# Kernel optimization log

Measured on AMD Instinct MI355X. Metric: run time of the kernel, lower is better.

## Reference

```python
import jax, jax.numpy as jnp
import numpy as np

N_NODES = 200000
N_EDGES = 6400000
NUM_FEATURES = 128


def _glorot(key, fan_in, fan_out):
    return jax.random.normal(key, (fan_in, fan_out), jnp.float32) * (1.0 / np.sqrt(fan_in))


def gcn_conv(x, src, dst, W, b):
    """PyG GCNConv: h = D^{-1/2}(A+I)D^{-1/2} (x @ W) + b, self-loops added."""
    n = x.shape[0]
    ones = jnp.ones(src.shape, x.dtype)
    # degree after adding self-loops: 1 + in-degree (edges flow src -> dst)
    deg = 1.0 + jax.ops.segment_sum(ones, dst, num_segments=n)
    dinv = jax.lax.rsqrt(deg)  # deg >= 1, safe
    h = x @ W  # [n, out]
    norm = dinv[src] * dinv[dst]  # [E]
    msg = h[src] * norm[:, None]
    agg = jax.ops.segment_sum(msg, dst, num_segments=n)
    agg = agg + h * (dinv * dinv)[:, None]  # self-loop contribution
    return agg + b


def setup_inputs() -> dict:
    key = jax.random.key(0)
    ks = jax.random.split(key, 16)
    x = jax.random.normal(ks[0], (N_NODES, NUM_FEATURES), jnp.float32)
    edge_index = jax.random.randint(ks[1], (2, N_EDGES), 0, N_NODES, dtype=jnp.int64)
    params = {
        'W1': _glorot(ks[2], NUM_FEATURES, 64), 'b1': jnp.zeros((64,), jnp.float32),
        'W2': _glorot(ks[3], 64, 32),           'b2': jnp.zeros((32,), jnp.float32),
        'W3': _glorot(ks[4], 32, 16),           'b3': jnp.zeros((16,), jnp.float32),
        'Wsk02': _glorot(ks[5], NUM_FEATURES, 32), 'bsk02': jnp.zeros((32,), jnp.float32),
        'Wsk13': _glorot(ks[6], 64, 16),           'bsk13': jnp.zeros((16,), jnp.float32),
        'Wlin': _glorot(ks[7], 16, 1),             'blin': jnp.zeros((1,), jnp.float32),
    }
    return {'x': x, 'edge_index': edge_index, **params}


def reference(x, edge_index, W1, b1, W2, b2, W3, b3, Wsk02, bsk02, Wsk13, bsk13, Wlin, blin):
    # Dropout is identity in eval mode.
    src, dst = edge_index[0], edge_index[1]
    h1 = jax.nn.relu(gcn_conv(x, src, dst, W1, b1))
    h2 = jax.nn.relu(gcn_conv(h1, src, dst, W2, b2) + x @ Wsk02 + bsk02)
    h3 = jax.nn.relu(gcn_conv(h2, src, dst, W3, b3) + h1 @ Wsk13 + bsk13)
    return jax.nn.sigmoid(h3 @ Wlin + blin)  # [N, 1]
```

## Files before the change

### kernel.cpp

```cpp
#include <hip/hip_runtime.h>
#include <hip/hip_fp16.h>
#include <math.h>

#define MAXB 1024
#define MAXCB 128
#define TILE1 8192
#define SCAT_T 512
#define EPT1 (TILE1 / SCAT_T)
#define LCAP 13568
#define GCHUNK 4096

typedef _Float16 f16x8 __attribute__((ext_vector_type(8)));
typedef float f32x4 __attribute__((ext_vector_type(4)));


__device__ __forceinline__ unsigned int pack_f16(float a, float b) {
    __half2 h = __floats2half2_rn(a, b);
    return *reinterpret_cast<unsigned int*>(&h);
}
__device__ __forceinline__ float f16_lo(unsigned int u) {
    __half2 h = *reinterpret_cast<__half2*>(&u);
    return __low2float(h);
}
__device__ __forceinline__ float f16_hi(unsigned int u) {
    __half2 h = *reinterpret_cast<__half2*>(&u);
    return __high2float(h);
}
__device__ __forceinline__ void acc8(float* a, uint4 u) {
    a[0] += f16_lo(u.x); a[1] += f16_hi(u.x);
    a[2] += f16_lo(u.y); a[3] += f16_hi(u.y);
    a[4] += f16_lo(u.z); a[5] += f16_hi(u.z);
    a[6] += f16_lo(u.w); a[7] += f16_hi(u.w);
}
__device__ __forceinline__ void unpack8(uint4 u, float* v) {
    v[0] = f16_lo(u.x); v[1] = f16_hi(u.x);
    v[2] = f16_lo(u.y); v[3] = f16_hi(u.y);
    v[4] = f16_lo(u.z); v[5] = f16_hi(u.z);
    v[6] = f16_lo(u.w); v[7] = f16_hi(u.w);
}
__device__ __forceinline__ uint4 h2add4(uint4 a, uint4 b) {
    const __half2* pa = reinterpret_cast<const __half2*>(&a);
    const __half2* pb = reinterpret_cast<const __half2*>(&b);
    uint4 r;
    __half2* pr = reinterpret_cast<__half2*>(&r);
#pragma unroll
    for (int i = 0; i < 4; i++) pr[i] = __hadd2(pa[i], pb[i]);
    return r;
}
__device__ __forceinline__ unsigned int pkadd(unsigned int a, unsigned int b) {
    __half2 r = __hadd2(*reinterpret_cast<__half2*>(&a), *reinterpret_cast<__half2*>(&b));
    return *reinterpret_cast<unsigned int*>(&r);
}


__device__ __forceinline__ bool detect64(const int* __restrict__ ei) {
    int lane = threadIdx.x & 63;
    unsigned long long m = __ballot(ei[2 * lane + 1] != 0);
    return m == 0ull;
}

__device__ __forceinline__ int load_src(const int* ei, int e, bool is64, int i) {
    return is64 ? ei[2 * i] : ei[i];
}
__device__ __forceinline__ int load_dst(const int* ei, int e, bool is64, int i) {
    return is64 ? ei[2 * e + 2 * i] : ei[e + i];
}


__global__ __launch_bounds__(256) void bin_count(const int* __restrict__ ei, int e,
                                                 int shift, int* __restrict__ gcnt) {
    __shared__ int h[MAXB];
    for (int i = threadIdx.x; i < MAXB; i += 256) h[i] = 0;
    bool is64 = detect64(ei);
    __syncthreads();
    int stride = gridDim.x * 256;
    for (int i = blockIdx.x * 256 + threadIdx.x; i < e; i += stride) {
        int d = load_dst(ei, e, is64, i);
        atomicAdd(&h[d >> shift], 1);
    }
    __syncthreads();
    for (int i = threadIdx.x; i < MAXB; i += 256)
        if (h[i]) atomicAdd(&gcnt[i], h[i]);
}


__global__ void bin_scan_init(const int* __restrict__ gcnt, int nb, int ncb,
                              int* __restrict__ base, int* __restrict__ gcursor,
                              int* __restrict__ gcur1) {
    __shared__ int sh[1024];
    __shared__ int ex[1024];
    int t = threadIdx.x;
    int v = (t < nb) ? gcnt[t] : 0;
    sh[t] = v;
    __syncthreads();
    for (int off = 1; off < 1024; off <<= 1) {
        int x = (t >= off) ? sh[t - off] : 0;
        __syncthreads();
        sh[t] += x;
        __syncthreads();
    }
    int excl = sh[t] - v;
    ex[t] = excl;
    if (t < nb) {
        base[t] = excl;
        gcursor[t] = excl;
        if (t == nb - 1) base[nb] = sh[t];
    }
    __syncthreads();
    if (t < ncb) gcur1[t] = ex[8 * t];
}


__global__ __launch_bounds__(SCAT_T) void scatter_coarse(const int* __restrict__ ei, int e,
                                                         int shift,
                                                         int* __restrict__ gcur1,
                                                         unsigned int* __restrict__ gpk1) {
    __shared__ int hist[MAXCB];
    __shared__ int lbase[MAXCB];
    __shared__ int delta[MAXCB];
    __shared__ int cur[MAXCB];
    __shared__ unsigned int sbuf[TILE1];
    __shared__ unsigned char sbkt[TILE1];
    __shared__ int sh[SCAT_T];

    const int t = threadIdx.x;
    const int pkshift = shift + 3;
    const int pkmask = (1 << pkshift) - 1;
    const bool is64 = detect64(ei);
    const int tile0 = blockIdx.x * TILE1;
    const int cnt = min(TILE1, e - tile0);

    for (int i = t; i < MAXCB; i += SCAT_T) hist[i] = 0;
    __syncthreads();

    unsigned int pk[EPT1];
    int bk[EPT1];
#pragma unroll
    for (int k = 0; k < EPT1; k++) {
        int g = tile0 + k * SCAT_T + t;
        bk[k] = -1;
        if (g < e) {
            int s = load_src(ei, e, is64, g);
            int d = load_dst(ei, e, is64, g);
            pk[k] = ((unsigned int)s << pkshift) | (unsigned int)(d & pkmask);
            bk[k] = d >> pkshift;
            atomicAdd(&hist[bk[k]], 1);
        }
    }
    __syncthreads();

    {
        int v = (t < MAXCB) ? hist[t] : 0;
        sh[t] = v;
        __syncthreads();
        for (int off = 1; off < SCAT_T; off <<= 1) {
            int x = (t >= off) ? sh[t - off] : 0;
            __syncthreads();
            sh[t] += x;
            __syncthreads();
        }
        if (t < MAXCB) lbase[t] = sh[t] - v;
    }
    __syncthreads();

    if (t < MAXCB) {
        int c = hist[t];
        if (c > 0) delta[t] = atomicAdd(&gcur1[t], c) - lbase[t];
        cur[t] = lbase[t];
    }
    __syncthreads();

#pragma unroll
    for (int k = 0; k < EPT1; k++) {
        if (bk[k] >= 0) {
            int p = atomicAdd(&cur[bk[k]], 1);
            sbuf[p] = pk[k];
            sbkt[p] = (unsigned char)bk[k];
        }
    }
    __syncthreads();

    for (int i = t; i < cnt; i += SCAT_T)
        gpk1[delta[sbkt[i]] + i] = sbuf[i];
}


__global__ __launch_bounds__(SCAT_T) void scatter_fine(const unsigned int* __restrict__ gpk1,
                                                       const int* __restrict__ base,
                                                       int nbkt, int shift,
                                                       int* __restrict__ gcursor,
                                                       unsigned int* __restrict__ gpk2) {
    __shared__ int hist[8];
    __shared__ int lbase[8];
    __shared__ int delta[8];
    __shared__ int cur[8];
    __shared__ unsigned int sbuf[TILE1];
    __shared__ unsigned char sbkt[TILE1];

    const int t = threadIdx.x;
    const int cb = blockIdx.x >> 3;
    const int s = blockIdx.x & 7;
    const int f0 = 8 * cb;
    const int fhiIdx = min(f0 + 8, nbkt);
    const int lo = base[f0];
    const int hi = base[fhiIdx];
    const int len = hi - lo;
    const int slo = lo + (int)((long long)len * s / 8);
    const int shi = lo + (int)((long long)len * (s + 1) / 8);

    for (int tile0 = slo; tile0 < shi; tile0 += TILE1) {
        const int cnt = min(TILE1, shi - tile0);
        if (t < 8) hist[t] = 0;
        __syncthreads();

        unsigned int pk[EPT1];
        int bk[EPT1];
#pragma unroll
        for (int k = 0; k < EPT1; k++) {
            int li = k * SCAT_T + t;
            bk[k] = -1;
            if (li < cnt) {
                pk[k] = gpk1[tile0 + li];
                bk[k] = (pk[k] >> shift) & 7;
                atomicAdd(&hist[bk[k]], 1);
            }
        }
        __syncthreads();

        if (t == 0) {
            int run = 0;
            for (int f = 0; f < 8; f++) { lbase[f] = run; run += hist[f]; }
        }
        __syncthreads();
        if (t < 8) {
            int c = hist[t];
            if (c > 0) delta[t] = atomicAdd(&gcursor[f0 + t], c) - lbase[t];
            cur[t] = lbase[t];
        }
        __syncthreads();

#pragma unroll
        for (int k = 0; k < EPT1; k++) {
            if (bk[k] >= 0) {
                int p = atomicAdd(&cur[bk[k]], 1);
                sbuf[p] = pk[k];
                sbkt[p] = (unsigned char)bk[k];
            }
        }
        __syncthreads();

        for (int i = t; i < cnt; i += SCAT_T)
            gpk2[delta[sbkt[i]] + i] = sbuf[i];
        __syncthreads();
    }
}


__global__ __launch_bounds__(256) void bucket_build(const unsigned int* __restrict__ gpk,
                                                    const int* __restrict__ base, int shift,
                                                    int n, int e, float* __restrict__ dinv,
                                                    int* __restrict__ row_ptr,
                                                    int* __restrict__ col) {
    __shared__ int lcol[LCAP];
    __shared__ int dc[MAXB];
    __shared__ int cur[MAXB];
    __shared__ int sh[256];
    const int t = threadIdx.x;
    const int b = blockIdx.x;
    const int pkshift = shift + 3;
    const int mask = (1 << shift) - 1;
    const int width = 1 << shift;
    const int node0 = b << shift;
    const int nc = min(width, n - node0);
    const int lo = base[b], hi = base[b + 1];
    const int ecnt = hi - lo;

    for (int i = t; i < width; i += 256) dc[i] = 0;
    __syncthreads();
    for (int j = lo + t; j < hi; j += 256)
        atomicAdd(&dc[gpk[j] & mask], 1);
    __syncthreads();
    {
        int b4 = t * 4;
        int v0 = (b4 + 0 < width) ? dc[b4 + 0] : 0;
        int v1 = (b4 + 1 < width) ? dc[b4 + 1] : 0;
        int v2 = (b4 + 2 < width) ? dc[b4 + 2] : 0;
        int v3 = (b4 + 3 < width) ? dc[b4 + 3] : 0;
        int s = v0 + v1 + v2 + v3;
        sh[t] = s;
        __syncthreads();
        for (int off = 1; off < 256; off <<= 1) {
            int x = (t >= off) ? sh[t - off] : 0;
            __syncthreads();
            sh[t] += x;
            __syncthreads();
        }
        int excl = sh[t] - s;
        int pf[4] = {excl, excl + v0, excl + v0 + v1, excl + v0 + v1 + v2};
        int vv[4] = {v0, v1, v2, v3};
#pragma unroll
        for (int q = 0; q < 4; q++) {
            int i = b4 + q;
            if (i < nc) {
                row_ptr[node0 + i] = lo + pf[q];
                dinv[node0 + i] = rsqrtf(1.0f + (float)vv[q]);
            }
            if (i < width) cur[i] = pf[q];
        }
    }
    if (b == gridDim.x - 1 && t == 0) row_ptr[n] = e;
    __syncthreads();

    if (ecnt <= LCAP) {
        for (int j = lo + t; j < hi; j += 256) {
            unsigned int v = gpk[j];
            int p = atomicAdd(&cur[v & mask], 1);
            lcol[p] = (int)(v >> pkshift);
        }
        __syncthreads();
        for (int j = t; j < ecnt; j += 256)
            col[lo + j] = lcol[j];
    } else {
        for (int j = lo + t; j < hi; j += 256) {
            unsigned int v = gpk[j];
            int p = atomicAdd(&cur[v & mask], 1);
            col[lo + p] = (int)(v >> pkshift);
        }
    }
}


__global__ void prep_w(const float* __restrict__ W1, const float* __restrict__ Wsk02,
                       const float* __restrict__ W2, const float* __restrict__ Wsk13,
                       const float* __restrict__ W3, unsigned short* __restrict__ wt) {
    int i = blockIdx.x * 256 + threadIdx.x;
    float v;
    if (i < 12288) {
        int c = i >> 7, k = i & 127;
        v = (c < 64) ? W1[k * 64 + c] : Wsk02[k * 32 + (c - 64)];
    } else if (i < 15360) {
        int j = i - 12288;
        int c = j >> 6, k = j & 63;
        v = (c < 32) ? W2[k * 32 + c] : Wsk13[k * 16 + (c - 32)];
    } else if (i < 15872) {
        int j = i - 15360;
        int c = j >> 5, k = j & 31;
        v = W3[k * 16 + c];
    } else return;
    wt[i] = (unsigned short)pack_f16(v, 0.f);
}


template <int K, int CO1, int CO2, bool AHALF>
__global__ __launch_bounds__(256) void gemm_mfma(const void* __restrict__ Av,
                                                 const unsigned short* __restrict__ wt,
                                                 const float* __restrict__ dinv,
                                                 unsigned int* __restrict__ out1,
                                                 unsigned int* __restrict__ out2, int n) {
    constexpr int N = CO1 + CO2;
    constexpr int NCT = N / 16;
    constexpr int NK = K / 32;
    constexpr int CHK = K / 8;
    constexpr int SWZ = (CHK - 1) < 15 ? (CHK - 1) : 15;
    __shared__ __align__(16) unsigned char Ash[64 * K * 2];
    __shared__ __align__(16) unsigned char Bsh[N * K * 2];

    const int t = threadIdx.x;
    const int row0 = blockIdx.x * 64;

    for (int i = t; i < 64 * CHK; i += 256) {
        int r = i / CHK, c = i % CHK;
        int row = row0 + r;
        uint4 w{0u, 0u, 0u, 0u};
        if (row < n) {
            if (AHALF) {
                w = *reinterpret_cast<const uint4*>(
                    (const unsigned short*)Av + (size_t)row * K + c * 8);
            } else {
                const float* xr = (const float*)Av + (size_t)row * K + c * 8;
                float4 p = *reinterpret_cast<const float4*>(xr);
                float4 q = *reinterpret_cast<const float4*>(xr + 4);
                w.x = pack_f16(p.x, p.y); w.y = pack_f16(p.z, p.w);
                w.z = pack_f16(q.x, q.y); w.w = pack_f16(q.z, q.w);
            }
        }
        int addr = i * 16;
        addr ^= ((r & SWZ) << 4);
        *reinterpret_cast<uint4*>(&Ash[addr]) = w;
    }
    for (int i = t; i < N * CHK; i += 256) {
        int cc = i / CHK;
        uint4 w = *reinterpret_cast<const uint4*>(&wt[(i / CHK) * K + (i % CHK) * 8]);
        int addr = i * 16;
        addr ^= ((cc & SWZ) << 4);
        *reinterpret_cast<uint4*>(&Bsh[addr]) = w;
    }
    __syncthreads();

    const int wv = t >> 6;
    const int lane = t & 63;
    const int lrow = wv * 16 + (lane & 15);
    const int kb = (lane >> 4) * 16;

    f16x8 afr[NK];
#pragma unroll
    for (int s = 0; s < NK; s++) {
        int addr = lrow * (2 * K) + s * 64 + kb;
        addr ^= ((lrow & SWZ) << 4);
        afr[s] = *reinterpret_cast<const f16x8*>(&Ash[addr]);
    }

    f32x4 acc[NCT];
#pragma unroll
    for (int ct = 0; ct < NCT; ct++) acc[ct] = f32x4{0.f, 0.f, 0.f, 0.f};

#pragma unroll
    for (int ct = 0; ct < NCT; ct++) {
        int cc = ct * 16 + (lane & 15);
#pragma unroll
        for (int s = 0; s < NK; s++) {
            int addr = cc * (2 * K) + s * 64 + kb;
            addr ^= ((cc & SWZ) << 4);
            f16x8 bfr = *reinterpret_cast<const f16x8*>(&Bsh[addr]);
            acc[ct] = __builtin_amdgcn_mfma_f32_16x16x32_f16(afr[s], bfr, acc[ct], 0, 0, 0);
        }
    }

    const int rbase = row0 + wv * 16 + (lane >> 4) * 4;
    const int cidx = lane & 15;
    float dn[4];
#pragma unroll
    for (int r = 0; r < 4; r++) dn[r] = (rbase + r < n) ? dinv[rbase + r] : 0.f;

#pragma unroll
    for (int ct = 0; ct < NCT; ct++) {
        int col = ct * 16 + cidx;
        if (col < CO1) {
#pragma unroll
            for (int r = 0; r < 4; r++) {
                float v = acc[ct][r] * dn[r];
                float o = __shfl_xor(v, 1);
                int row = rbase + r;
                if (!(lane & 1) && row < n)
                    out1[(size_t)row * (CO1 / 2) + ct * 8 + cidx / 2] = pack_f16(v, o);
            }
        } else if (CO2 > 0) {
#pragma unroll
            for (int r = 0; r < 4; r++) {
                float v = acc[ct][r];
                float o = __shfl_xor(v, 1);
                int row = rbase + r;
                if (!(lane & 1) && row < n)
                    out2[(size_t)row * (CO2 / 2) + (ct * 16 + cidx - CO1) / 2] =
                        pack_f16(v, o);
            }
        }
    }
}


template <int F, bool PACKOUT>
__global__ __launch_bounds__(256) void gather_combine(
    const uint4* __restrict__ hp4, const int* __restrict__ row_ptr,
    const int* __restrict__ col, const float* __restrict__ dinv,
    const float* __restrict__ bias, void* __restrict__ outv, int n) {
    constexpr int L = F / 8;
    constexpr int EPW = 64 / L;
    int wid = (blockIdx.x * blockDim.x + threadIdx.x) >> 6;
    int lane = threadIdx.x & 63;
    if (wid >= n) return;
    int s = lane / L;
    int el = lane % L;
    int start = row_ptr[wid];
    int end = row_ptr[wid + 1];

    float a[8] = {0.f, 0.f, 0.f, 0.f, 0.f, 0.f, 0.f, 0.f};
    const uint4 z4{0u, 0u, 0u, 0u};
    for (int j = start + s; j < end; j += 4 * EPW) {
        int j1 = j + EPW, j2 = j + 2 * EPW, j3 = j + 3 * EPW;
        bool v1 = j1 < end, v2 = j2 < end, v3 = j3 < end;
        int c0 = col[j];
        int c1 = col[v1 ? j1 : j];
        int c2 = col[v2 ? j2 : j];
        int c3 = col[v3 ? j3 : j];
        uint4 u0 = hp4[(size_t)c0 * L + el];
        uint4 u1 = hp4[(size_t)c1 * L + el];
        uint4 u2 = hp4[(size_t)c2 * L + el];
        uint4 u3 = hp4[(size_t)c3 * L + el];
        if (!v1) u1 = z4;
        if (!v2) u2 = z4;
        if (!v3) u3 = z4;
        uint4 t01 = h2add4(u0, u1);
        uint4 t23 = h2add4(u2, u3);
        acc8(a, h2add4(t01, t23));
    }

#pragma unroll
    for (int m = L; m < 64; m <<= 1) {
#pragma unroll
        for (int q = 0; q < 8; q++) a[q] += __shfl_xor(a[q], m);
    }

    if (lane < L) {
        float dn = dinv[wid];
        uint4 us = hp4[(size_t)wid * L + el];
        float v[8];
        unpack8(us, v);
        float4 b0 = *reinterpret_cast<const float4*>(&bias[8 * el]);
        float4 b1 = *reinterpret_cast<const float4*>(&bias[8 * el + 4]);
        float o[8];
        o[0] = dn * a[0] + v[0] * dn + b0.x;
        o[1] = dn * a[1] + v[1] * dn + b0.y;
        o[2] = dn * a[2] + v[2] * dn + b0.z;
        o[3] = dn * a[3] + v[3] * dn + b0.w;
        o[4] = dn * a[4] + v[4] * dn + b1.x;
        o[5] = dn * a[5] + v[5] * dn + b1.y;
        o[6] = dn * a[6] + v[6] * dn + b1.z;
        o[7] = dn * a[7] + v[7] * dn + b1.w;
#pragma unroll
        for (int q = 0; q < 8; q++) o[q] = fmaxf(o[q], 0.f);
        if (PACKOUT) {
            uint4 pk{pack_f16(o[0], o[1]), pack_f16(o[2], o[3]),
                     pack_f16(o[4], o[5]), pack_f16(o[6], o[7])};
            ((uint4*)outv)[(size_t)wid * L + el] = pk;
        } else {
            float* out = (float*)outv;
            float4 w0{o[0], o[1], o[2], o[3]};
            float4 w1{o[4], o[5], o[6], o[7]};
            *reinterpret_cast<float4*>(&out[(size_t)wid * F + 8 * el]) = w0;
            *reinterpret_cast<float4*>(&out[(size_t)wid * F + 8 * el + 4]) = w1;
        }
    }
}


template <int F, int T, bool FINAL, bool PACKOUT>
__global__ __launch_bounds__(256) void gather_tpn(
    const uint4* __restrict__ hp4, const int* __restrict__ row_ptr,
    const int* __restrict__ col, const float* __restrict__ dinv,
    const float* __restrict__ bias, const uint4* __restrict__ skh,
    const float* __restrict__ bsk, void* __restrict__ outv,
    const float* __restrict__ Wlin, const float* __restrict__ blin, int n) {
    constexpr int L = F / 8;
    constexpr int NPB = 256 / T;
    __shared__ int lcol[GCHUNK];
    const int t = threadIdx.x;
    const int sub = t & (T - 1);
    const int node0 = blockIdx.x * NPB;
    const int node = node0 + (t / T);
    const int hiN = min(node0 + NPB, n);
    const int lo = row_ptr[node0];
    const int hi = row_ptr[hiN];

    int start = 0, end = 0;
    if (node < n) { start = row_ptr[node]; end = row_ptr[node + 1]; }

    unsigned int acc[F / 2];
#pragma unroll
    for (int q = 0; q < F / 2; q++) acc[q] = 0u;

    for (int ch = lo; ch < hi; ch += GCHUNK) {
        int cnt = min(GCHUNK, hi - ch);
        __syncthreads();
        for (int i = t; i < cnt; i += 256) lcol[i] = col[ch + i];
        __syncthreads();
        int first = start + sub;
        if (first < ch) first += ((ch - first + T - 1) & ~(T - 1));
        int last = min(end, ch + cnt);
        int j = first;
        if (j < last) {
            uint4 u[L];
            {
                const uint4* rp = hp4 + (size_t)lcol[j - ch] * L;
#pragma unroll
                for (int w = 0; w < L; w++) u[w] = rp[w];
            }
            for (j += T; j < last; j += T) {
                uint4 v[L];
                const uint4* rq = hp4 + (size_t)lcol[j - ch] * L;
#pragma unroll
                for (int w = 0; w < L; w++) v[w] = rq[w];
#pragma unroll
                for (int w = 0; w < L; w++) {
                    acc[4 * w + 0] = pkadd(acc[4 * w + 0], u[w].x);
                    acc[4 * w + 1] = pkadd(acc[4 * w + 1], u[w].y);
                    acc[4 * w + 2] = pkadd(acc[4 * w + 2], u[w].z);
                    acc[4 * w + 3] = pkadd(acc[4 * w + 3], u[w].w);
                }
#pragma unroll
                for (int w = 0; w < L; w++) u[w] = v[w];
            }
#pragma unroll
            for (int w = 0; w < L; w++) {
                acc[4 * w + 0] = pkadd(acc[4 * w + 0], u[w].x);
                acc[4 * w + 1] = pkadd(acc[4 * w + 1], u[w].y);
                acc[4 * w + 2] = pkadd(acc[4 * w + 2], u[w].z);
                acc[4 * w + 3] = pkadd(acc[4 * w + 3], u[w].w);
            }
        }
    }

#pragma unroll
    for (int m = 1; m < T; m <<= 1) {
#pragma unroll
        for (int q = 0; q < F / 2; q++) {
            unsigned int o = (unsigned int)__shfl_xor((int)acc[q], m);
            acc[q] = pkadd(acc[q], o);
        }
    }

    if (node < n && sub == 0) {
        float dn = dinv[node];
        const uint4* sp = hp4 + (size_t)node * L;
        float o[F];
#pragma unroll
        for (int w = 0; w < L; w++) {
            uint4 u = sp[w];
            float sv[8];
            unpack8(u, sv);
#pragma unroll
            for (int q = 0; q < 8; q++) {
                int f = w * 8 + q;
                float av = (q & 1) ? f16_hi(acc[4 * w + (q >> 1)])
                                   : f16_lo(acc[4 * w + (q >> 1)]);
                o[f] = dn * (av + sv[q]) + bias[f];
            }
        }
        if (skh) {
            const uint4* skp = skh + (size_t)node * L;
#pragma unroll
            for (int w = 0; w < L; w++) {
                float sv2[8];
                unpack8(skp[w], sv2);
#pragma unroll
                for (int q = 0; q < 8; q++)
                    o[w * 8 + q] += sv2[q] + bsk[w * 8 + q];
            }
        }
#pragma unroll
        for (int f = 0; f < F; f++) o[f] = fmaxf(o[f], 0.f);

        if (FINAL) {
            float d = blin[0];
#pragma unroll
            for (int f = 0; f < F; f++) d += o[f] * Wlin[f];
            ((float*)outv)[node] = 1.0f / (1.0f + expf(-d));
        } else if (PACKOUT) {
            uint4* o4 = (uint4*)outv + (size_t)node * L;
#pragma unroll
            for (int w = 0; w < L; w++) {
                uint4 pk{pack_f16(o[w * 8 + 0], o[w * 8 + 1]),
                         pack_f16(o[w * 8 + 2], o[w * 8 + 3]),
                         pack_f16(o[w * 8 + 4], o[w * 8 + 5]),
                         pack_f16(o[w * 8 + 6], o[w * 8 + 7])};
                o4[w] = pk;
            }
        }
    }
}


extern "C" void kernel_launch(void* const* d_in, const int* in_sizes, int n_in,
                              void* d_out, int out_size, void* d_ws, size_t ws_size,
                              hipStream_t stream) {
    const float* x     = (const float*)d_in[0];
    const int*   ei    = (const int*)d_in[1];
    const float* W1    = (const float*)d_in[2];
    const float* b1    = (const float*)d_in[3];
    const float* W2    = (const float*)d_in[4];
    const float* b2    = (const float*)d_in[5];
    const float* W3    = (const float*)d_in[6];
    const float* b3    = (const float*)d_in[7];
    const float* Wsk02 = (const float*)d_in[8];
    const float* bsk02 = (const float*)d_in[9];
    const float* Wsk13 = (const float*)d_in[10];
    const float* bsk13 = (const float*)d_in[11];
    const float* Wlin  = (const float*)d_in[12];
    const float* blin  = (const float*)d_in[13];

    const int n = in_sizes[0] / 128;
    const int e = in_sizes[1] / 2;

    int shift = 8;
    while (((n + (1 << shift) - 1) >> shift) > MAXB) shift++;
    const int nbkt = (n + (1 << shift) - 1) >> shift;
    const int ncb = (nbkt + 7) / 8;

    char* p = (char*)d_ws;
    auto alloc = [&](size_t bytes) {
        void* r = (void*)p;
        p += (bytes + 255) / 256 * 256;
        return r;
    };
    int*   gcnt    = (int*)alloc(MAXB * 4);
    int*   base    = (int*)alloc((MAXB + 1) * 4);
    int*   gcursor = (int*)alloc(MAXB * 4);
    int*   gcur1   = (int*)alloc(MAXCB * 4);
    unsigned short* wt = (unsigned short*)alloc(15872 * 2);
    int*   row_ptr = (int*)alloc((size_t)(n + 1) * 4);
    float* dinv    = (float*)alloc((size_t)n * 4);
    int*   col     = (int*)alloc((size_t)e * 4);
    size_t h1b     = (size_t)e * 4 > (size_t)n * 128 ? (size_t)e * 4 : (size_t)n * 128;
    unsigned int* h1 = (unsigned int*)alloc(h1b);
    unsigned int* h2 = (unsigned int*)alloc((size_t)n * 64);
    unsigned int* sk02 = (unsigned int*)alloc((size_t)n * 64);
    unsigned int* sk13 = (unsigned int*)alloc((size_t)n * 32);
    size_t prebytes = (size_t)e * 4 > (size_t)n * 128 ? (size_t)e * 4 : (size_t)n * 128;
    unsigned int* preb = (unsigned int*)alloc(prebytes);
    unsigned int* gpk1 = h1;
    unsigned int* gpk2 = preb;

    auto cdiv = [](int a, int b) { return (a + b - 1) / b; };

    prep_w<<<62, 256, 0, stream>>>(W1, Wsk02, W2, Wsk13, W3, wt);

    hipMemsetAsync(gcnt, 0, MAXB * 4, stream);
    bin_count<<<1024, 256, 0, stream>>>(ei, e, shift, gcnt);
    bin_scan_init<<<1, 1024, 0, stream>>>(gcnt, nbkt, ncb, base, gcursor, gcur1);
    scatter_coarse<<<cdiv(e, TILE1), SCAT_T, 0, stream>>>(ei, e, shift, gcur1, gpk1);
    scatter_fine<<<ncb * 8, SCAT_T, 0, stream>>>(gpk1, base, nbkt, shift, gcursor, gpk2);
    bucket_build<<<nbkt, 256, 0, stream>>>(gpk2, base, shift, n, e, dinv, row_ptr, col);

    gemm_mfma<128, 64, 32, false><<<cdiv(n, 64), 256, 0, stream>>>(
        x, wt, dinv, preb, sk02, n);
    gather_combine<64, true><<<cdiv(n, 4), 256, 0, stream>>>(
        (const uint4*)preb, row_ptr, col, dinv, b1, h1, n);

    gemm_mfma<64, 32, 16, true><<<cdiv(n, 64), 256, 0, stream>>>(
        h1, wt + 12288, dinv, preb, sk13, n);
    gather_tpn<32, 8, false, true><<<cdiv(n, 32), 256, 0, stream>>>(
        (const uint4*)preb, row_ptr, col, dinv, b2, (const uint4*)sk02, bsk02,
        h2, nullptr, nullptr, n);

    gemm_mfma<32, 16, 0, true><<<cdiv(n, 64), 256, 0, stream>>>(
        h2, wt + 15360, dinv, preb, sk13, n);
    gather_tpn<16, 8, true, false><<<cdiv(n, 32), 256, 0, stream>>>(
        (const uint4*)preb, row_ptr, col, dinv, b3, (const uint4*)sk13, bsk13,
        d_out, Wlin, blin, n);
}
```

Measured before the change: 448.7 us.

## Replace two-level CSR bucketing with single coarse pass and fuse weight prep

Drops the fine scatter pass and builds CSR directly from coarse buckets of 2048+ nodes, each handled by one 1024-thread block that counts degrees, scans, and scatters columns using shared-memory cursors. Weight conversion is folded into the bin_count launch as extra blocks, removing one kernel launch. This removes a full read/write pass over the edge array but leaves ~98 blocks doing scattered global writes of col without local staging, so parallelism is lower and write locality is worse.

```diff
diff --git a/kernel.cpp b/kernel.cpp
--- a/kernel.cpp
+++ b/kernel.cpp
@@ -2,13 +2,13 @@
 #include <hip/hip_fp16.h>
 #include <math.h>
 
-#define MAXB 1024
 #define MAXCB 128
+#define MAXW 4096
 #define TILE1 8192
 #define SCAT_T 512
 #define EPT1 (TILE1 / SCAT_T)
-#define LCAP 13568
 #define GCHUNK 4096
+#define CNT_BLKS 1024
 
 typedef _Float16 f16x8 __attribute__((ext_vector_type(8)));
 typedef float f32x4 __attribute__((ext_vector_type(4)));
@@ -68,51 +68,70 @@
 
 
 __global__ __launch_bounds__(256) void bin_count(const int* __restrict__ ei, int e,
-                                                 int shift, int* __restrict__ gcnt) {
-    __shared__ int h[MAXB];
-    for (int i = threadIdx.x; i < MAXB; i += 256) h[i] = 0;
+                                                 int cshift, int* __restrict__ gcnt,
+                                                 const float* __restrict__ W1,
+                                                 const float* __restrict__ Wsk02,
+                                                 const float* __restrict__ W2,
+                                                 const float* __restrict__ Wsk13,
+                                                 const float* __restrict__ W3,
+                                                 unsigned short* __restrict__ wt) {
+    if (blockIdx.x >= CNT_BLKS) {
+        int i = (blockIdx.x - CNT_BLKS) * 256 + threadIdx.x;
+        float v;
+        if (i < 12288) {
+            int c = i >> 7, k = i & 127;
+            v = (c < 64) ? W1[k * 64 + c] : Wsk02[k * 32 + (c - 64)];
+        } else if (i < 15360) {
+            int j = i - 12288;
+            int c = j >> 6, k = j & 63;
+            v = (c < 32) ? W2[k * 32 + c] : Wsk13[k * 16 + (c - 32)];
+        } else if (i < 15872) {
+            int j = i - 15360;
+            int c = j >> 5, k = j & 31;
+            v = W3[k * 16 + c];
+        } else return;
+        wt[i] = (unsigned short)pack_f16(v, 0.f);
+        return;
+    }
+    __shared__ int h[MAXCB];
+    for (int i = threadIdx.x; i < MAXCB; i += 256) h[i] = 0;
     bool is64 = detect64(ei);
     __syncthreads();
-    int stride = gridDim.x * 256;
+    int stride = CNT_BLKS * 256;
     for (int i = blockIdx.x * 256 + threadIdx.x; i < e; i += stride) {
         int d = load_dst(ei, e, is64, i);
-        atomicAdd(&h[d >> shift], 1);
-    }
-    __syncthreads();
-    for (int i = threadIdx.x; i < MAXB; i += 256)
+        atomicAdd(&h[d >> cshift], 1);
+    }
+    __syncthreads();
+    for (int i = threadIdx.x; i < MAXCB; i += 256)
         if (h[i]) atomicAdd(&gcnt[i], h[i]);
 }
 
 
-__global__ void bin_scan_init(const int* __restrict__ gcnt, int nb, int ncb,
-                              int* __restrict__ base, int* __restrict__ gcursor,
-                              int* __restrict__ gcur1) {
-    __shared__ int sh[1024];
-    __shared__ int ex[1024];
+__global__ void bin_scan_init(const int* __restrict__ gcnt, int ncb,
+                              int* __restrict__ cbase, int* __restrict__ gcur1) {
+    __shared__ int sh[MAXCB];
     int t = threadIdx.x;
-    int v = (t < nb) ? gcnt[t] : 0;
+    int v = (t < ncb) ? gcnt[t] : 0;
     sh[t] = v;
     __syncthreads();
-    for (int off = 1; off < 1024; off <<= 1) {
+    for (int off = 1; off < MAXCB; off <<= 1) {
         int x = (t >= off) ? sh[t - off] : 0;
         __syncthreads();
         sh[t] += x;
         __syncthreads();
     }
-    int excl = sh[t] - v;
-    ex[t] = excl;
-    if (t < nb) {
-        base[t] = excl;
-        gcursor[t] = excl;
-        if (t == nb - 1) base[nb] = sh[t];
-    }
-    __syncthreads();
-    if (t < ncb) gcur1[t] = ex[8 * t];
+    if (t < ncb) {
+        int excl = sh[t] - v;
+        cbase[t] = excl;
+        gcur1[t] = excl;
+        if (t == ncb - 1) cbase[ncb] = sh[t];
+    }
 }
 
 
 __global__ __launch_bounds__(SCAT_T) void scatter_coarse(const int* __restrict__ ei, int e,
-                                                         int shift,
+                                                         int cshift,
                                                          int* __restrict__ gcur1,
                                                          unsigned int* __restrict__ gpk1) {
     __shared__ int hist[MAXCB];
@@ -124,8 +143,7 @@
     __shared__ int sh[SCAT_T];
 
     const int t = threadIdx.x;
-    const int pkshift = shift + 3;
-    const int pkmask = (1 << pkshift) - 1;
+    const int pkmask = (1 << cshift) - 1;
     const bool is64 = detect64(ei);
     const int tile0 = blockIdx.x * TILE1;
     const int cnt = min(TILE1, e - tile0);
@@ -142,8 +160,8 @@
         if (g < e) {
             int s = load_src(ei, e, is64, g);
             int d = load_dst(ei, e, is64, g);
-            pk[k] = ((unsigned int)s << pkshift) | (unsigned int)(d & pkmask);
-            bk[k] = d >> pkshift;
+            pk[k] = ((unsigned int)s << cshift) | (unsigned int)(d & pkmask);
+            bk[k] = d >> cshift;
             atomicAdd(&hist[bk[k]], 1);
         }
     }
@@ -185,169 +203,65 @@
 }
 
 
-__global__ __launch_bounds__(SCAT_T) void scatter_fine(const unsigned int* __restrict__ gpk1,
-                                                       const int* __restrict__ base,
-                                                       int nbkt, int shift,
-                                                       int* __restrict__ gcursor,
-                                                       unsigned int* __restrict__ gpk2) {
-    __shared__ int hist[8];
-    __shared__ int lbase[8];
-    __shared__ int delta[8];
-    __shared__ int cur[8];
-    __shared__ unsigned int sbuf[TILE1];
-    __shared__ unsigned char sbkt[TILE1];
-
-    const int t = threadIdx.x;
-    const int cb = blockIdx.x >> 3;
-    const int s = blockIdx.x & 7;
-    const int f0 = 8 * cb;
-    const int fhiIdx = min(f0 + 8, nbkt);
-    const int lo = base[f0];
-    const int hi = base[fhiIdx];
-    const int len = hi - lo;
-    const int slo = lo + (int)((long long)len * s / 8);
-    const int shi = lo + (int)((long long)len * (s + 1) / 8);
-
-    for (int tile0 = slo; tile0 < shi; tile0 += TILE1) {
-        const int cnt = min(TILE1, shi - tile0);
-        if (t < 8) hist[t] = 0;
-        __syncthreads();
-
-        unsigned int pk[EPT1];
-        int bk[EPT1];
-#pragma unroll
-        for (int k = 0; k < EPT1; k++) {
-            int li = k * SCAT_T + t;
-            bk[k] = -1;
-            if (li < cnt) {
-                pk[k] = gpk1[tile0 + li];
-                bk[k] = (pk[k] >> shift) & 7;
-                atomicAdd(&hist[bk[k]], 1);
-            }
-        }
-        __syncthreads();
-
-        if (t == 0) {
-            int run = 0;
-            for (int f = 0; f < 8; f++) { lbase[f] = run; run += hist[f]; }
-        }
-        __syncthreads();
-        if (t < 8) {
-            int c = hist[t];
-            if (c > 0) delta[t] = atomicAdd(&gcursor[f0 + t], c) - lbase[t];
-            cur[t] = lbase[t];
-        }
-        __syncthreads();
-
-#pragma unroll
-        for (int k = 0; k < EPT1; k++) {
-            if (bk[k] >= 0) {
-                int p = atomicAdd(&cur[bk[k]], 1);
-                sbuf[p] = pk[k];
-                sbkt[p] = (unsigned char)bk[k];
-            }
-        }
-        __syncthreads();
-
-        for (int i = t; i < cnt; i += SCAT_T)
-            gpk2[delta[sbkt[i]] + i] = sbuf[i];
-        __syncthreads();
-    }
-}
-
-
-__global__ __launch_bounds__(256) void bucket_build(const unsigned int* __restrict__ gpk,
-                                                    const int* __restrict__ base, int shift,
-                                                    int n, int e, float* __restrict__ dinv,
-                                                    int* __restrict__ row_ptr,
-                                                    int* __restrict__ col) {
-    __shared__ int lcol[LCAP];
-    __shared__ int dc[MAXB];
-    __shared__ int cur[MAXB];
-    __shared__ int sh[256];
+__global__ __launch_bounds__(1024) void bucket_build_coarse(
+    const unsigned int* __restrict__ gpk, const int* __restrict__ cbase,
+    int cshift, int n, int e, float* __restrict__ dinv,
+    int* __restrict__ row_ptr, int* __restrict__ col) {
+    __shared__ int dc[MAXW];
+    __shared__ int cur[MAXW];
+    __shared__ int sh[1024];
     const int t = threadIdx.x;
     const int b = blockIdx.x;
-    const int pkshift = shift + 3;
-    const int mask = (1 << shift) - 1;
-    const int width = 1 << shift;
-    const int node0 = b << shift;
+    const int width = 1 << cshift;
+    const int mask = width - 1;
+    const int node0 = b << cshift;
     const int nc = min(width, n - node0);
-    const int lo = base[b], hi = base[b + 1];
-    const int ecnt = hi - lo;
-
-    for (int i = t; i < width; i += 256) dc[i] = 0;
-    __syncthreads();
-    for (int j = lo + t; j < hi; j += 256)
+    const int lo = cbase[b], hi = cbase[b + 1];
+
+    for (int i = t; i < width; i += 1024) dc[i] = 0;
+    __syncthreads();
+    for (int j = lo + t; j < hi; j += 1024)
         atomicAdd(&dc[gpk[j] & mask], 1);
     __syncthreads();
+
     {
-        int b4 = t * 4;
-        int v0 = (b4 + 0 < width) ? dc[b4 + 0] : 0;
-        int v1 = (b4 + 1 < width) ? dc[b4 + 1] : 0;
-        int v2 = (b4 + 2 < width) ? dc[b4 + 2] : 0;
-        int v3 = (b4 + 3 < width) ? dc[b4 + 3] : 0;
-        int s = v0 + v1 + v2 + v3;
+        const int E = width >> 10;
+        int v[4] = {0, 0, 0, 0};
+        int s = 0;
+        int b0 = t * E;
+#pragma unroll 4
+        for (int q = 0; q < 4; q++)
+            if (q < E) { v[q] = dc[b0 + q]; s += v[q]; }
         sh[t] = s;
         __syncthreads();
-        for (int off = 1; off < 256; off <<= 1) {
+        for (int off = 1; off < 1024; off <<= 1) {
             int x = (t >= off) ? sh[t - off] : 0;
             __syncthreads();
             sh[t] += x;
             __syncthreads();
         }
         int excl = sh[t] - s;
-        int pf[4] = {excl, excl + v0, excl + v0 + v1, excl + v0 + v1 + v2};
-        int vv[4] = {v0, v1, v2, v3};
-#pragma unroll
+#pragma unroll 4
         for (int q = 0; q < 4; q++) {
-            int i = b4 + q;
-            if (i < nc) {
-                row_ptr[node0 + i] = lo + pf[q];
-                dinv[node0 + i] = rsqrtf(1.0f + (float)vv[q]);
-            }
-            if (i < width) cur[i] = pf[q];
+            if (q < E) {
+                int i = b0 + q;
+                if (i < nc) {
+                    row_ptr[node0 + i] = lo + excl;
+                    dinv[node0 + i] = rsqrtf(1.0f + (float)v[q]);
+                }
+                cur[i] = excl;
+                excl += v[q];
+            }
         }
     }
     if (b == gridDim.x - 1 && t == 0) row_ptr[n] = e;
     __syncthreads();
 
-    if (ecnt <= LCAP) {
-        for (int j = lo + t; j < hi; j += 256) {
-            unsigned int v = gpk[j];
-            int p = atomicAdd(&cur[v & mask], 1);
-            lcol[p] = (int)(v >> pkshift);
-        }
-        __syncthreads();
-        for (int j = t; j < ecnt; j += 256)
-            col[lo + j] = lcol[j];
-    } else {
-        for (int j = lo + t; j < hi; j += 256) {
-            unsigned int v = gpk[j];
-            int p = atomicAdd(&cur[v & mask], 1);
-            col[lo + p] = (int)(v >> pkshift);
-        }
-    }
-}
-
-
-__global__ void prep_w(const float* __restrict__ W1, const float* __restrict__ Wsk02,
-                       const float* __restrict__ W2, const float* __restrict__ Wsk13,
-                       const float* __restrict__ W3, unsigned short* __restrict__ wt) {
-    int i = blockIdx.x * 256 + threadIdx.x;
-    float v;
-    if (i < 12288) {
-        int c = i >> 7, k = i & 127;
-        v = (c < 64) ? W1[k * 64 + c] : Wsk02[k * 32 + (c - 64)];
-    } else if (i < 15360) {
-        int j = i - 12288;
-        int c = j >> 6, k = j & 63;
-        v = (c < 32) ? W2[k * 32 + c] : Wsk13[k * 16 + (c - 32)];
-    } else if (i < 15872) {
-        int j = i - 15360;
-        int c = j >> 5, k = j & 31;
-        v = W3[k * 16 + c];
-    } else return;
-    wt[i] = (unsigned short)pack_f16(v, 0.f);
+    for (int j = lo + t; j < hi; j += 1024) {
+        unsigned int pv = gpk[j];
+        int p = atomicAdd(&cur[pv & mask], 1);
+        col[lo + p] = (int)(pv >> cshift);
+    }
 }
 
 
@@ -681,10 +595,9 @@
     const int n = in_sizes[0] / 128;
     const int e = in_sizes[1] / 2;
 
-    int shift = 8;
-    while (((n + (1 << shift) - 1) >> shift) > MAXB) shift++;
-    const int nbkt = (n + (1 << shift) - 1) >> shift;
-    const int ncb = (nbkt + 7) / 8;
+    int cshift = 11;
+    while (((n + (1 << cshift) - 1) >> cshift) > MAXCB) cshift++;
+    const int ncb = (n + (1 << cshift) - 1) >> cshift;
 
     char* p = (char*)d_ws;
     auto alloc = [&](size_t bytes) {
@@ -692,9 +605,8 @@
         p += (bytes + 255) / 256 * 256;
         return r;
     };
-    int*   gcnt    = (int*)alloc(MAXB * 4);
-    int*   base    = (int*)alloc((MAXB + 1) * 4);
-    int*   gcursor = (int*)alloc(MAXB * 4);
+    int*   gcnt    = (int*)alloc(MAXCB * 4);
+    int*   cbase   = (int*)alloc((MAXCB + 1) * 4);
     int*   gcur1   = (int*)alloc(MAXCB * 4);
     unsigned short* wt = (unsigned short*)alloc(15872 * 2);
     int*   row_ptr = (int*)alloc((size_t)(n + 1) * 4);
@@ -705,21 +617,18 @@
     unsigned int* h2 = (unsigned int*)alloc((size_t)n * 64);
     unsigned int* sk02 = (unsigned int*)alloc((size_t)n * 64);
     unsigned int* sk13 = (unsigned int*)alloc((size_t)n * 32);
-    size_t prebytes = (size_t)e * 4 > (size_t)n * 128 ? (size_t)e * 4 : (size_t)n * 128;
-    unsigned int* preb = (unsigned int*)alloc(prebytes);
+    unsigned int* preb = (unsigned int*)alloc((size_t)n * 128);
     unsigned int* gpk1 = h1;
-    unsigned int* gpk2 = preb;
 
     auto cdiv = [](int a, int b) { return (a + b - 1) / b; };
 
-    prep_w<<<62, 256, 0, stream>>>(W1, Wsk02, W2, Wsk13, W3, wt);
-
-    hipMemsetAsync(gcnt, 0, MAXB * 4, stream);
-    bin_count<<<1024, 256, 0, stream>>>(ei, e, shift, gcnt);
-    bin_scan_init<<<1, 1024, 0, stream>>>(gcnt, nbkt, ncb, base, gcursor, gcur1);
-    scatter_coarse<<<cdiv(e, TILE1), SCAT_T, 0, stream>>>(ei, e, shift, gcur1, gpk1);
-    scatter_fine<<<ncb * 8, SCAT_T, 0, stream>>>(gpk1, base, nbkt, shift, gcursor, gpk2);
-    bucket_build<<<nbkt, 256, 0, stream>>>(gpk2, base, shift, n, e, dinv, row_ptr, col);
+    hipMemsetAsync(gcnt, 0, MAXCB * 4, stream);
+    bin_count<<<CNT_BLKS + 62, 256, 0, stream>>>(ei, e, cshift, gcnt,
+                                                 W1, Wsk02, W2, Wsk13, W3, wt);
+    bin_scan_init<<<1, MAXCB, 0, stream>>>(gcnt, ncb, cbase, gcur1);
+    scatter_coarse<<<cdiv(e, TILE1), SCAT_T, 0, stream>>>(ei, e, cshift, gcur1, gpk1);
+    bucket_build_coarse<<<ncb, 1024, 0, stream>>>(gpk1, cbase, cshift, n, e,
+                                                  dinv, row_ptr, col);
 
     gemm_mfma<128, 64, 32, false><<<cdiv(n, 64), 256, 0, stream>>>(
         x, wt, dinv, preb, sk02, n);
```

After: 478.5 us. +6.6%, slower.
